# Performance work log

Hardware: AMD Instinct MI355X
Metric: run time of the kernel (lower is better)

## Reference

```python
import jax, jax.numpy as jnp
import numpy as np

B, T, I, H = 64, 1024, 128, 512

def setup_inputs() -> dict:
    key = jax.random.key(0)
    ks = jax.random.split(key, 7)
    s_ih = 1.0 / np.sqrt(H)
    return {
        "x": jax.random.normal(ks[0], (B, T, I), dtype=jnp.float32),
        "W_ih": jax.random.uniform(ks[1], (H, I), minval=-s_ih, maxval=s_ih, dtype=jnp.float32),
        "W_hh": jax.random.uniform(ks[2], (H, H), minval=-s_ih, maxval=s_ih, dtype=jnp.float32),
        "b_ih": jax.random.uniform(ks[3], (H,), minval=-s_ih, maxval=s_ih, dtype=jnp.float32),
        "b_hh": jax.random.uniform(ks[4], (H,), minval=-s_ih, maxval=s_ih, dtype=jnp.float32),
        "fc_w": jax.random.uniform(ks[5], (1, H), minval=-s_ih, maxval=s_ih, dtype=jnp.float32),
        "fc_b": jax.random.uniform(ks[6], (1,), minval=-s_ih, maxval=s_ih, dtype=jnp.float32),
    }

def reference(x, W_ih, W_hh, b_ih, b_hh, fc_w, fc_b):
    # Precompute input projection for all timesteps: [B,T,H]
    xp = jnp.einsum('bti,hi->bth', x, W_ih) + b_ih + b_hh

    def step(h, xp_t):
        # h: [B,H], xp_t: [B,H]
        h_new = jnp.tanh(xp_t + h @ W_hh.T)
        return h_new, None

    h0 = jnp.zeros((B, H), dtype=x.dtype)
    h_last, _ = jax.lax.scan(step, h0, jnp.swapaxes(xp, 0, 1))  # scan over T
    # final linear head: [B,1]
    return h_last @ fc_w.T + fc_b
```

## Files before the change

### kernel.cpp

```cpp
#include <hip/hip_runtime.h>
#include <math.h>

#define B_ 64
#define T_ 1024
#define I_ 128
#define H_ 512

typedef _Float16 h2_t __attribute__((ext_vector_type(2)));
union U32H2 { unsigned u; h2_t h; };

__device__ __forceinline__ float fdot2u(unsigned a, unsigned b, float c) {
    U32H2 ua, ub; ua.u = a; ub.u = b;
    return __builtin_amdgcn_fdot2(ua.h, ub.h, c, false);
}
__device__ __forceinline__ unsigned packh2(float x, float y) {
    U32H2 r; r.h.x = (_Float16)x; r.h.y = (_Float16)y; return r.u;
}

__global__ void prep(const float* __restrict__ wih, const float* __restrict__ whh,
                     const float* __restrict__ bih, const float* __restrict__ bhh,
                     unsigned* __restrict__ wpack, unsigned* __restrict__ wldsg,
                     unsigned* __restrict__ wih2, float* __restrict__ biasv) {
    int e = blockIdx.x * 256 + threadIdx.x;
    if (e < 512 * 192) {
        int tid = e / 192, r = e % 192;
        int j = r / 48, kk2 = r % 48;
        int c = tid >> 7, g = tid & 127;
        int row = (g << 2) + j;
        int col = (c << 7) + (kk2 << 1);
        wpack[e] = packh2(whh[row * H_ + col], whh[row * H_ + col + 1]);
    }
    if (e < 4 * 16 * 512) {
        int c = e >> 13, m = (e >> 9) & 15, col = e & 511;
        int k = (c << 7) + 96 + (m << 1);
        wldsg[e] = packh2(whh[col * H_ + k], whh[col * H_ + k + 1]);
    }
    if (e < 64 * 512) {
        int i2 = e >> 9, h = e & 511;
        wih2[e] = packh2(wih[h * I_ + (i2 << 1)], wih[h * I_ + (i2 << 1) + 1]);
    }
    if (e < H_) biasv[e] = bih[e] + bhh[e];
}

__global__ __launch_bounds__(512, 2) void xp_gemm(
    const float* __restrict__ x, const unsigned* __restrict__ wih2,
    const float* __restrict__ biasv, _Float16* __restrict__ xph) {
    __shared__ unsigned w2[64 * 512];
    __shared__ unsigned x2[32 * 64];
    const int tid = threadIdx.x, b = blockIdx.x, t0 = blockIdx.y * 32;

    #pragma unroll
    for (int q = 0; q < 64; ++q) w2[tid + (q << 9)] = wih2[tid + (q << 9)];
    #pragma unroll
    for (int q = 0; q < 4; ++q) {
        int idx = tid * 4 + q;
        int t = idx >> 6, i2 = idx & 63;
        const float2 xv = *(const float2*)(x + ((size_t)b * T_ + t0 + t) * I_ + (i2 << 1));
        x2[idx] = packh2(xv.x, xv.y);
    }
    __syncthreads();
    const float bias = biasv[tid];
    for (int t = 0; t < 32; ++t) {
        float acc = bias;
        #pragma unroll
        for (int i2 = 0; i2 < 64; ++i2)
            acc = fdot2u(x2[(t << 6) + i2], w2[(i2 << 9) + tid], acc);
        xph[((size_t)b * T_ + t0 + t) * H_ + tid] = (_Float16)acc;
    }
}

__global__ __launch_bounds__(512) void rnn_fused(
    const unsigned* __restrict__ xp2,
    const unsigned* __restrict__ wpack,
    const unsigned* __restrict__ wldsg,
    const float* __restrict__ fcw, const float* __restrict__ fcb,
    float* __restrict__ out)
{
    __shared__ __align__(16) unsigned wlds[4 * 16 * 512];
    __shared__ __align__(16) float part[4 * 512];
    __shared__ __align__(16) unsigned h2buf[256];
    __shared__ float wsum[4];

    const int tid = threadIdx.x;
    const int b = blockIdx.x;
    const int c = tid >> 7, g = tid & 127;

    {
        const uint4* src = (const uint4*)wldsg;
        uint4* dst = (uint4*)wlds;
        #pragma unroll
        for (int q = 0; q < 16; ++q) dst[tid + (q << 9)] = src[tid + (q << 9)];
    }
    unsigned wreg[4][48];
    {
        const unsigned* wp = wpack + tid * 192;
        #pragma unroll
        for (int j = 0; j < 4; ++j)
            #pragma unroll
            for (int kk2 = 0; kk2 < 48; ++kk2)
                wreg[j][kk2] = wp[j * 48 + kk2];
    }
    if (tid < 256) h2buf[tid] = 0u;
    __syncthreads();

    const unsigned* xpb = xp2 + (size_t)b * T_ * 256;
    const uint4* wq = ((const uint4*)wlds) + (c << 11) + g;
    const uint4* hv = ((const uint4*)h2buf) + (c << 4);
    float4* part4w = ((float4*)part) + (c << 7) + g;
    const float2* p2 = (const float2*)part;

    unsigned xpw = (tid < 256) ? xpb[tid] : 0u;

    for (int t = 0; t < T_; ++t) {
        unsigned xpn = 0u;
        if (tid < 256 && t + 1 < T_) xpn = xpb[(t + 1) * 256 + tid];

        float a0 = 0.f, a1 = 0.f, a2 = 0.f, a3 = 0.f;
        #pragma unroll
        for (int q = 0; q < 12; ++q) {
            const uint4 hh = hv[q];
            const int m = q << 2;
            a0 = fdot2u(wreg[0][m+0], hh.x, a0); a1 = fdot2u(wreg[1][m+0], hh.x, a1);
            a2 = fdot2u(wreg[2][m+0], hh.x, a2); a3 = fdot2u(wreg[3][m+0], hh.x, a3);
            a0 = fdot2u(wreg[0][m+1], hh.y, a0); a1 = fdot2u(wreg[1][m+1], hh.y, a1);
            a2 = fdot2u(wreg[2][m+1], hh.y, a2); a3 = fdot2u(wreg[3][m+1], hh.y, a3);
            a0 = fdot2u(wreg[0][m+2], hh.z, a0); a1 = fdot2u(wreg[1][m+2], hh.z, a1);
            a2 = fdot2u(wreg[2][m+2], hh.z, a2); a3 = fdot2u(wreg[3][m+2], hh.z, a3);
            a0 = fdot2u(wreg[0][m+3], hh.w, a0); a1 = fdot2u(wreg[1][m+3], hh.w, a1);
            a2 = fdot2u(wreg[2][m+3], hh.w, a2); a3 = fdot2u(wreg[3][m+3], hh.w, a3);
        }
        #pragma unroll
        for (int q = 0; q < 4; ++q) {
            const uint4 hh = hv[12 + q];
            const uint4 w0 = wq[(q * 4 + 0) * 128];
            const uint4 w1 = wq[(q * 4 + 1) * 128];
            const uint4 w2v = wq[(q * 4 + 2) * 128];
            const uint4 w3 = wq[(q * 4 + 3) * 128];
            a0 = fdot2u(w0.x, hh.x, a0); a1 = fdot2u(w0.y, hh.x, a1);
            a2 = fdot2u(w0.z, hh.x, a2); a3 = fdot2u(w0.w, hh.x, a3);
            a0 = fdot2u(w1.x, hh.y, a0); a1 = fdot2u(w1.y, hh.y, a1);
            a2 = fdot2u(w1.z, hh.y, a2); a3 = fdot2u(w1.w, hh.y, a3);
            a0 = fdot2u(w2v.x, hh.z, a0); a1 = fdot2u(w2v.y, hh.z, a1);
            a2 = fdot2u(w2v.z, hh.z, a2); a3 = fdot2u(w2v.w, hh.z, a3);
            a0 = fdot2u(w3.x, hh.w, a0); a1 = fdot2u(w3.y, hh.w, a1);
            a2 = fdot2u(w3.z, hh.w, a2); a3 = fdot2u(w3.w, hh.w, a3);
        }
        *part4w = make_float4(a0, a1, a2, a3);
        __syncthreads();

        if (tid < 256) {
            float2 s0 = p2[tid];
            float2 s1 = p2[256 + tid];
            float2 s2 = p2[512 + tid];
            float2 s3 = p2[768 + tid];
            U32H2 xu; xu.u = xpw;
            float pre0 = (float)xu.h.x + s0.x + s1.x + s2.x + s3.x;
            float pre1 = (float)xu.h.y + s0.y + s1.y + s2.y + s3.y;
            float e0 = __expf(2.0f * pre0), e1 = __expf(2.0f * pre1);
            float h0 = 1.0f - 2.0f / (e0 + 1.0f);
            float h1 = 1.0f - 2.0f / (e1 + 1.0f);
            h2buf[tid] = packh2(h0, h1);
        }
        xpw = xpn;
        __syncthreads();
    }

    float p = 0.f;
    if (tid < 256) {
        U32H2 hu; hu.u = h2buf[tid];
        p = (float)hu.h.x * fcw[tid << 1] + (float)hu.h.y * fcw[(tid << 1) + 1];
    }
    #pragma unroll
    for (int off = 32; off >= 1; off >>= 1) p += __shfl_down(p, off, 64);
    if ((tid & 63) == 0 && tid < 256) wsum[tid >> 6] = p;
    __syncthreads();
    if (tid == 0) out[b] = wsum[0] + wsum[1] + wsum[2] + wsum[3] + fcb[0];
}

extern "C" void kernel_launch(void* const* d_in, const int* in_sizes, int n_in,
                              void* d_out, int out_size, void* d_ws, size_t ws_size,
                              hipStream_t stream) {
    const float* x   = (const float*)d_in[0];
    const float* wih = (const float*)d_in[1];
    const float* whh = (const float*)d_in[2];
    const float* bih = (const float*)d_in[3];
    const float* bhh = (const float*)d_in[4];
    const float* fcw = (const float*)d_in[5];
    const float* fcb = (const float*)d_in[6];
    float* out = (float*)d_out;

    unsigned* xp2   = (unsigned*)d_ws;
    unsigned* wpack = xp2 + 16777216;
    unsigned* wldsg = wpack + 98304;
    unsigned* wih2  = wldsg + 32768;
    float*    biasv = (float*)(wih2 + 32768);

    hipLaunchKernelGGL(prep, dim3(384), dim3(256), 0, stream,
                       wih, whh, bih, bhh, wpack, wldsg, wih2, biasv);
    hipLaunchKernelGGL(xp_gemm, dim3(B_, 32), dim3(512), 0, stream,
                       x, wih2, biasv, (_Float16*)xp2);
    hipLaunchKernelGGL(rnn_fused, dim3(B_), dim3(512), 0, stream,
                       xp2, wpack, wldsg, fcw, fcb, out);
}
```

Before: 1.631 ms.

## Split recurrent matvec across 1024 threads with eight-way K partitioning

The recurrent kernel now launches 1024 threads per batch row instead of 512. The hidden dimension of each step's matvec is split into eight chunks instead of four, so each thread holds half as many register-resident W_hh weights and does half the dot-product work per timestep. The prep kernel repacks the weights into a uint4-strided layout so the register and LDS loads are coalesced. The cost is an eight-way partial-sum reduction through a larger LDS buffer and about 128 VGPRs available per thread, which could cause spills.

Measured after the change: 1.762 ms. 8.0% more time.

```diff
diff --git a/kernel.cpp b/kernel.cpp
--- a/kernel.cpp
+++ b/kernel.cpp
@@ -22,18 +22,22 @@
                      unsigned* __restrict__ wpack, unsigned* __restrict__ wldsg,
                      unsigned* __restrict__ wih2, float* __restrict__ biasv) {
     int e = blockIdx.x * 256 + threadIdx.x;
-    if (e < 512 * 192) {
-        int tid = e / 192, r = e % 192;
-        int j = r / 48, kk2 = r % 48;
+    if (e < 98304) {
+        int u4 = e >> 2, r4 = e & 3;
+        int qr = u4 >> 10, tid = u4 & 1023;
+        int r = qr / 6, q = qr % 6;
+        int m = (q << 2) + r4;
         int c = tid >> 7, g = tid & 127;
-        int row = (g << 2) + j;
-        int col = (c << 7) + (kk2 << 1);
-        wpack[e] = packh2(whh[row * H_ + col], whh[row * H_ + col + 1]);
-    }
-    if (e < 4 * 16 * 512) {
-        int c = e >> 13, m = (e >> 9) & 15, col = e & 511;
-        int k = (c << 7) + 96 + (m << 1);
-        wldsg[e] = packh2(whh[col * H_ + k], whh[col * H_ + k + 1]);
+        int j = (g << 2) + r;
+        int w = (c << 5) + m;
+        wpack[e] = packh2(whh[j * H_ + 2 * w], whh[j * H_ + 2 * w + 1]);
+    }
+    if (e < 32768) {
+        int u = e >> 2, r = e & 3;
+        int c = u >> 10, mp = (u >> 7) & 7, g = u & 127;
+        int j = (g << 2) + r;
+        int w = (c << 5) + 24 + mp;
+        wldsg[e] = packh2(whh[j * H_ + 2 * w], whh[j * H_ + 2 * w + 1]);
     }
     if (e < 64 * 512) {
         int i2 = e >> 9, h = e & 511;
@@ -69,15 +73,15 @@
     }
 }
 
-__global__ __launch_bounds__(512) void rnn_fused(
+__global__ __launch_bounds__(1024) void rnn_fused(
     const unsigned* __restrict__ xp2,
     const unsigned* __restrict__ wpack,
     const unsigned* __restrict__ wldsg,
     const float* __restrict__ fcw, const float* __restrict__ fcb,
     float* __restrict__ out)
 {
-    __shared__ __align__(16) unsigned wlds[4 * 16 * 512];
-    __shared__ __align__(16) float part[4 * 512];
+    __shared__ __align__(16) unsigned wlds[32768];
+    __shared__ __align__(16) float part[8 * 512];
     __shared__ __align__(16) unsigned h2buf[256];
     __shared__ float wsum[4];
 
@@ -89,73 +93,73 @@
         const uint4* src = (const uint4*)wldsg;
         uint4* dst = (uint4*)wlds;
         #pragma unroll
-        for (int q = 0; q < 16; ++q) dst[tid + (q << 9)] = src[tid + (q << 9)];
-    }
-    unsigned wreg[4][48];
+        for (int q = 0; q < 8; ++q) dst[tid + (q << 10)] = src[tid + (q << 10)];
+    }
+    uint4 wr[4][6];
     {
-        const unsigned* wp = wpack + tid * 192;
-        #pragma unroll
-        for (int j = 0; j < 4; ++j)
+        const uint4* wp4 = ((const uint4*)wpack) + tid;
+        #pragma unroll
+        for (int r = 0; r < 4; ++r)
             #pragma unroll
-            for (int kk2 = 0; kk2 < 48; ++kk2)
-                wreg[j][kk2] = wp[j * 48 + kk2];
+            for (int q = 0; q < 6; ++q)
+                wr[r][q] = wp4[(r * 6 + q) << 10];
     }
     if (tid < 256) h2buf[tid] = 0u;
     __syncthreads();
 
     const unsigned* xpb = xp2 + (size_t)b * T_ * 256;
-    const uint4* wq = ((const uint4*)wlds) + (c << 11) + g;
-    const uint4* hv = ((const uint4*)h2buf) + (c << 4);
-    float4* part4w = ((float4*)part) + (c << 7) + g;
+    const uint4* hv  = ((const uint4*)h2buf) + (c << 3);
+    const uint4* wqp = ((const uint4*)wlds) + (c << 10) + g;
+    float4* pw = ((float4*)part) + (c << 7) + g;
     const float2* p2 = (const float2*)part;
 
     unsigned xpw = (tid < 256) ? xpb[tid] : 0u;
 
     for (int t = 0; t < T_; ++t) {
-        unsigned xpn = 0u;
-        if (tid < 256 && t + 1 < T_) xpn = xpb[(t + 1) * 256 + tid];
+        unsigned xpn = (tid < 256) ? xpb[(t + 1) * 256 + tid] : 0u;
 
         float a0 = 0.f, a1 = 0.f, a2 = 0.f, a3 = 0.f;
         #pragma unroll
-        for (int q = 0; q < 12; ++q) {
+        for (int q = 0; q < 6; ++q) {
             const uint4 hh = hv[q];
-            const int m = q << 2;
-            a0 = fdot2u(wreg[0][m+0], hh.x, a0); a1 = fdot2u(wreg[1][m+0], hh.x, a1);
-            a2 = fdot2u(wreg[2][m+0], hh.x, a2); a3 = fdot2u(wreg[3][m+0], hh.x, a3);
-            a0 = fdot2u(wreg[0][m+1], hh.y, a0); a1 = fdot2u(wreg[1][m+1], hh.y, a1);
-            a2 = fdot2u(wreg[2][m+1], hh.y, a2); a3 = fdot2u(wreg[3][m+1], hh.y, a3);
-            a0 = fdot2u(wreg[0][m+2], hh.z, a0); a1 = fdot2u(wreg[1][m+2], hh.z, a1);
-            a2 = fdot2u(wreg[2][m+2], hh.z, a2); a3 = fdot2u(wreg[3][m+2], hh.z, a3);
-            a0 = fdot2u(wreg[0][m+3], hh.w, a0); a1 = fdot2u(wreg[1][m+3], hh.w, a1);
-            a2 = fdot2u(wreg[2][m+3], hh.w, a2); a3 = fdot2u(wreg[3][m+3], hh.w, a3);
+            a0 = fdot2u(wr[0][q].x, hh.x, a0); a1 = fdot2u(wr[1][q].x, hh.x, a1);
+            a2 = fdot2u(wr[2][q].x, hh.x, a2); a3 = fdot2u(wr[3][q].x, hh.x, a3);
+            a0 = fdot2u(wr[0][q].y, hh.y, a0); a1 = fdot2u(wr[1][q].y, hh.y, a1);
+            a2 = fdot2u(wr[2][q].y, hh.y, a2); a3 = fdot2u(wr[3][q].y, hh.y, a3);
+            a0 = fdot2u(wr[0][q].z, hh.z, a0); a1 = fdot2u(wr[1][q].z, hh.z, a1);
+            a2 = fdot2u(wr[2][q].z, hh.z, a2); a3 = fdot2u(wr[3][q].z, hh.z, a3);
+            a0 = fdot2u(wr[0][q].w, hh.w, a0); a1 = fdot2u(wr[1][q].w, hh.w, a1);
+            a2 = fdot2u(wr[2][q].w, hh.w, a2); a3 = fdot2u(wr[3][q].w, hh.w, a3);
         }
         #pragma unroll
-        for (int q = 0; q < 4; ++q) {
-            const uint4 hh = hv[12 + q];
-            const uint4 w0 = wq[(q * 4 + 0) * 128];
-            const uint4 w1 = wq[(q * 4 + 1) * 128];
-            const uint4 w2v = wq[(q * 4 + 2) * 128];
-            const uint4 w3 = wq[(q * 4 + 3) * 128];
-            a0 = fdot2u(w0.x, hh.x, a0); a1 = fdot2u(w0.y, hh.x, a1);
-            a2 = fdot2u(w0.z, hh.x, a2); a3 = fdot2u(w0.w, hh.x, a3);
-            a0 = fdot2u(w1.x, hh.y, a0); a1 = fdot2u(w1.y, hh.y, a1);
-            a2 = fdot2u(w1.z, hh.y, a2); a3 = fdot2u(w1.w, hh.y, a3);
-            a0 = fdot2u(w2v.x, hh.z, a0); a1 = fdot2u(w2v.y, hh.z, a1);
-            a2 = fdot2u(w2v.z, hh.z, a2); a3 = fdot2u(w2v.w, hh.z, a3);
-            a0 = fdot2u(w3.x, hh.w, a0); a1 = fdot2u(w3.y, hh.w, a1);
-            a2 = fdot2u(w3.z, hh.w, a2); a3 = fdot2u(w3.w, hh.w, a3);
+        for (int q = 0; q < 2; ++q) {
+            const uint4 hh = hv[6 + q];
+            {   const uint4 w0 = wqp[(q * 4 + 0) * 128];
+                a0 = fdot2u(w0.x, hh.x, a0); a1 = fdot2u(w0.y, hh.x, a1);
+                a2 = fdot2u(w0.z, hh.x, a2); a3 = fdot2u(w0.w, hh.x, a3); }
+            {   const uint4 w1 = wqp[(q * 4 + 1) * 128];
+                a0 = fdot2u(w1.x, hh.y, a0); a1 = fdot2u(w1.y, hh.y, a1);
+                a2 = fdot2u(w1.z, hh.y, a2); a3 = fdot2u(w1.w, hh.y, a3); }
+            {   const uint4 w2v = wqp[(q * 4 + 2) * 128];
+                a0 = fdot2u(w2v.x, hh.z, a0); a1 = fdot2u(w2v.y, hh.z, a1);
+                a2 = fdot2u(w2v.z, hh.z, a2); a3 = fdot2u(w2v.w, hh.z, a3); }
+            {   const uint4 w3 = wqp[(q * 4 + 3) * 128];
+                a0 = fdot2u(w3.x, hh.w, a0); a1 = fdot2u(w3.y, hh.w, a1);
+                a2 = fdot2u(w3.z, hh.w, a2); a3 = fdot2u(w3.w, hh.w, a3); }
         }
-        *part4w = make_float4(a0, a1, a2, a3);
+        *pw = make_float4(a0, a1, a2, a3);
         __syncthreads();
 
         if (tid < 256) {
-            float2 s0 = p2[tid];
-            float2 s1 = p2[256 + tid];
-            float2 s2 = p2[512 + tid];
-            float2 s3 = p2[768 + tid];
+            float sx = 0.f, sy = 0.f;
+            #pragma unroll
+            for (int cc = 0; cc < 8; ++cc) {
+                const float2 s = p2[(cc << 8) + tid];
+                sx += s.x; sy += s.y;
+            }
             U32H2 xu; xu.u = xpw;
-            float pre0 = (float)xu.h.x + s0.x + s1.x + s2.x + s3.x;
-            float pre1 = (float)xu.h.y + s0.y + s1.y + s2.y + s3.y;
+            float pre0 = (float)xu.h.x + sx;
+            float pre1 = (float)xu.h.y + sy;
             float e0 = __expf(2.0f * pre0), e1 = __expf(2.0f * pre1);
             float h0 = 1.0f - 2.0f / (e0 + 1.0f);
             float h1 = 1.0f - 2.0f / (e1 + 1.0f);
@@ -199,6 +203,6 @@
                        wih, whh, bih, bhh, wpack, wldsg, wih2, biasv);
     hipLaunchKernelGGL(xp_gemm, dim3(B_, 32), dim3(512), 0, stream,
                        x, wih2, biasv, (_Float16*)xp2);
-    hipLaunchKernelGGL(rnn_fused, dim3(B_), dim3(512), 0, stream,
+    hipLaunchKernelGGL(rnn_fused, dim3(B_), dim3(1024), 0, stream,
                        xp2, wpack, wldsg, fcw, fcb, out);
 }
```
